# Kernel optimization log

Measured on AMD Instinct MI355X. Metric: run time of the kernel, lower is better.

The kernel has to match this reference:

```python
import jax, jax.numpy as jnp
import numpy as np

B, H, W, C = 8, 64, 64, 256
NH, WS, SS = 8, 8, 4
HD = C // NH          # head dim 32
N = WS * WS           # 64 tokens per window
NW = (H // WS) * (W // WS)  # 64 windows
MLP = 4 * C


def _rel_index():
    ch = np.arange(WS)
    coords = np.stack(np.meshgrid(ch, ch, indexing='ij')).reshape(2, -1)  # [2, N]
    rel = (coords[:, :, None] - coords[:, None, :]).transpose(1, 2, 0)   # [N, N, 2]
    rel[:, :, 0] += WS - 1
    rel[:, :, 1] += WS - 1
    rel[:, :, 0] *= 2 * WS - 1
    return jnp.asarray(rel.sum(-1))  # [N, N] indices into table

REL_IDX = _rel_index()


def _attn_mask():
    # standard Swin shifted-window mask: [nW, N, N] with 0 / -100
    img = np.zeros((H, W))
    slices = (slice(0, -WS), slice(-WS, -SS), slice(-SS, None))
    cnt = 0
    for hs in slices:
        for ws_ in slices:
            img[hs, ws_] = cnt
            cnt += 1
    m = img.reshape(H // WS, WS, W // WS, WS).transpose(0, 2, 1, 3).reshape(-1, N)
    diff = m[:, None, :] - m[:, :, None]
    return jnp.asarray(np.where(diff != 0, -100.0, 0.0).astype(np.float32))

MASK = _attn_mask()


def setup_inputs() -> dict:
    key = jax.random.key(0)
    ks = jax.random.split(key, 8)
    s = 0.02
    return {
        'hidden_states': jax.random.normal(ks[0], (B, H * W, C), jnp.float32),
        'ln1_g': jnp.ones((C,), jnp.float32),
        'ln1_b': jnp.zeros((C,), jnp.float32),
        'wq': jax.random.normal(ks[1], (C, C), jnp.float32) * s,
        'bq': jnp.zeros((C,), jnp.float32),
        'wk': jax.random.normal(ks[2], (C, C), jnp.float32) * s,
        'bk': jnp.zeros((C,), jnp.float32),
        'wv': jax.random.normal(ks[3], (C, C), jnp.float32) * s,
        'bv': jnp.zeros((C,), jnp.float32),
        'rel_table': jax.random.normal(ks[4], ((2 * WS - 1) ** 2, NH), jnp.float32) * s,
        'wo': jax.random.normal(ks[5], (C, C), jnp.float32) * s,
        'bo': jnp.zeros((C,), jnp.float32),
        'ln2_g': jnp.ones((C,), jnp.float32),
        'ln2_b': jnp.zeros((C,), jnp.float32),
        'w1': jax.random.normal(ks[6], (MLP, C), jnp.float32) * s,
        'b1': jnp.zeros((MLP,), jnp.float32),
        'w2': jax.random.normal(ks[7], (C, MLP), jnp.float32) * s,
        'b2': jnp.zeros((C,), jnp.float32),
    }


def _ln(x, g, b):
    mu = x.mean(-1, keepdims=True)
    var = x.var(-1, keepdims=True)
    return (x - mu) * jax.lax.rsqrt(var + 1e-5) * g + b


def reference(hidden_states, ln1_g, ln1_b, wq, bq, wk, bk, wv, bv, rel_table,
              wo, bo, ln2_g, ln2_b, w1, b1, w2, b2):
    shortcut = hidden_states
    x = _ln(hidden_states, ln1_g, ln1_b).reshape(B, H, W, C)
    # cyclic shift
    x = jnp.roll(x, (-SS, -SS), axis=(1, 2))
    # window partition -> [B*nW, N, C]
    xw = x.reshape(B, H // WS, WS, W // WS, WS, C).transpose(0, 1, 3, 2, 4, 5).reshape(-1, N, C)
    q = (xw @ wq.T + bq).reshape(-1, N, NH, HD).transpose(0, 2, 1, 3)
    k = (xw @ wk.T + bk).reshape(-1, N, NH, HD).transpose(0, 2, 1, 3)
    v = (xw @ wv.T + bv).reshape(-1, N, NH, HD).transpose(0, 2, 1, 3)
    scores = jnp.einsum('bhnd,bhmd->bhnm', q, k) / np.float32(np.sqrt(HD))
    bias = rel_table[REL_IDX]                 # [N, N, NH] gathered bias
    scores = scores + bias.transpose(2, 0, 1)[None]
    scores = scores.reshape(B, NW, NH, N, N) + MASK[None, :, None]
    probs = jax.nn.softmax(scores, axis=-1).reshape(-1, NH, N, N)
    ctx = jnp.einsum('bhnm,bhmd->bnhd', probs, v).reshape(-1, N, C)
    attn_out = ctx @ wo.T + bo                # SelfOutput dense
    # window reverse + reverse shift
    x = attn_out.reshape(B, H // WS, W // WS, WS, WS, C).transpose(0, 1, 3, 2, 4, 5).reshape(B, H, W, C)
    x = jnp.roll(x, (SS, SS), axis=(1, 2)).reshape(B, H * W, C)
    hidden = shortcut + x
    y = _ln(hidden, ln2_g, ln2_b)
    y = jax.nn.gelu(y @ w1.T + b1, approximate=False) @ w2.T + b2
    return hidden + y
```

## Files before the change

### kernel.cpp

```cpp
#include <hip/hip_runtime.h>
#include <hip/hip_bf16.h>
#include <math.h>

__device__ __forceinline__ unsigned short f2bf(float f) {
    union { float f; unsigned u; } c; c.f = f;
    unsigned r = c.u + 0x7fffu + ((c.u >> 16) & 1u);
    return (unsigned short)(r >> 16);
}
__device__ __forceinline__ float bfu(unsigned short u) {
    union { unsigned x; float f; } c; c.x = ((unsigned)u) << 16; return c.f;
}
__device__ __forceinline__ float gelu_t(float x) {
    float z = x * (1.59576912f + 0.07135481f * x * x);
    return x / (1.0f + __expf(-z));
}

typedef __bf16 bf16x8_t __attribute__((ext_vector_type(8)));
typedef float  f32x4_t  __attribute__((ext_vector_type(4)));
typedef unsigned short u16x8 __attribute__((ext_vector_type(8)));

#define AS1 __attribute__((address_space(1)))
#define AS3 __attribute__((address_space(3)))
__device__ __forceinline__ void g2lds16(const void* g, void* l) {
    __builtin_amdgcn_global_load_lds((const AS1 unsigned int*)g, (AS3 unsigned int*)l, 16, 0, 0);
}

__global__ void cvt_all(const float* __restrict__ wq, const float* __restrict__ wk,
                        const float* __restrict__ wv, const float* __restrict__ wo,
                        const float* __restrict__ w1, const float* __restrict__ w2,
                        unsigned short* __restrict__ wqkv_b, unsigned short* __restrict__ wo_b,
                        unsigned short* __restrict__ w1_b, unsigned short* __restrict__ w2_b) {
    int i = blockIdx.x * 256 + threadIdx.x;
    const float* src; unsigned short* dst; int base;
    if (i < 16384)       { src = wq; dst = wqkv_b;          base = 0; }
    else if (i < 32768)  { src = wk; dst = wqkv_b + 65536;  base = 16384; }
    else if (i < 49152)  { src = wv; dst = wqkv_b + 131072; base = 32768; }
    else if (i < 65536)  { src = wo; dst = wo_b;            base = 49152; }
    else if (i < 131072) { src = w1; dst = w1_b;            base = 65536; }
    else                 { src = w2; dst = w2_b;            base = 131072; }
    int j = (i - base) * 4;
    float4 v = *(const float4*)(src + j);
    ushort4 o = { f2bf(v.x), f2bf(v.y), f2bf(v.z), f2bf(v.w) };
    *(ushort4*)(dst + j) = o;
}

template<int GATHER, int BF16IN>
__global__ void ln_kernel(const void* __restrict__ xv, const float* __restrict__ g,
                          const float* __restrict__ b, unsigned short* __restrict__ out) {
    int row  = blockIdx.x * 4 + (threadIdx.x >> 6);
    int lane = threadIdx.x & 63;
    int src;
    if (GATHER) {
        int bb = row >> 12;
        int rem = row & 4095;
        int winid = rem >> 6, tok = rem & 63;
        int wi = winid >> 3, wj = winid & 7;
        int ii = tok >> 3,  jj = tok & 7;
        int hh = (wi * 8 + ii + 4) & 63;
        int ww = (wj * 8 + jj + 4) & 63;
        src = (bb << 12) + hh * 64 + ww;
    } else {
        src = row;
    }
    float4 v;
    if (BF16IN) {
        ushort4 u = *(const ushort4*)((const unsigned short*)xv + (size_t)src * 256 + lane * 4);
        v.x = bfu(u.x); v.y = bfu(u.y); v.z = bfu(u.z); v.w = bfu(u.w);
    } else {
        v = *(const float4*)((const float*)xv + (size_t)src * 256 + lane * 4);
    }
    float s  = v.x + v.y + v.z + v.w;
    float s2 = v.x*v.x + v.y*v.y + v.z*v.z + v.w*v.w;
    #pragma unroll
    for (int off = 32; off > 0; off >>= 1) {
        s  += __shfl_xor(s,  off, 64);
        s2 += __shfl_xor(s2, off, 64);
    }
    float mean = s * (1.0f / 256.0f);
    float var  = s2 * (1.0f / 256.0f) - mean * mean;
    float rstd = rsqrtf(var + 1e-5f);
    int c0 = lane * 4;
    float4 gg  = *(const float4*)(g + c0);
    float4 bb4 = *(const float4*)(b + c0);
    ushort4 o;
    o.x = f2bf((v.x - mean) * rstd * gg.x + bb4.x);
    o.y = f2bf((v.y - mean) * rstd * gg.y + bb4.y);
    o.z = f2bf((v.z - mean) * rstd * gg.z + bb4.z);
    o.w = f2bf((v.w - mean) * rstd * gg.w + bb4.w);
    *(ushort4*)(out + (size_t)row * 256 + c0) = o;
}

template<int MODE, int K>
__global__ __launch_bounds__(256, 4) void gemm_tile(
        const unsigned short* __restrict__ A,
        const unsigned short* __restrict__ Bw,
        const float* __restrict__ bias,
        int M, int N,
        unsigned short* __restrict__ obf,
        float* __restrict__ of32,
        const void* __restrict__ addp) {
    __shared__ __align__(16) char smem_raw[64 * 132 * 4];
    unsigned short* As = (unsigned short*)smem_raw;
    unsigned short* Bs = As + 128 * 64;
    float* cst = (float*)smem_raw;
    const int t = threadIdx.x;
    const int lane = t & 63, wave = t >> 6;
    const int m0 = blockIdx.x * 128, n0 = blockIdx.y * 128;
    const int wm = (wave >> 1) * 64, wn = (wave & 1) * 64;
    const int lr = lane & 15, kg = lane >> 4;

    f32x4_t acc[4][4];
    #pragma unroll
    for (int i = 0; i < 4; ++i)
        #pragma unroll
        for (int j = 0; j < 4; ++j) { acc[i][j][0]=0.f; acc[i][j][1]=0.f; acc[i][j][2]=0.f; acc[i][j][3]=0.f; }

    const int srow = t >> 3;
    const int sck  = (t & 7) * 8;
    const unsigned short* ga = A  + (size_t)(m0 + srow) * K + sck;
    const unsigned short* gb = Bw + (size_t)(n0 + srow) * K + sck;
    unsigned short* la = &As[t * 8];
    unsigned short* lb = &Bs[t * 8];

    #pragma unroll
    for (int k0 = 0; k0 < K; k0 += 64) {
        __syncthreads();
        #pragma unroll
        for (int i = 0; i < 4; ++i) {
            g2lds16(ga + (size_t)(i * 32) * K + k0, la + i * 2048);
            g2lds16(gb + (size_t)(i * 32) * K + k0, lb + i * 2048);
        }
        __syncthreads();
        #pragma unroll
        for (int ks = 0; ks < 64; ks += 32) {
            bf16x8_t af[4], bfr[4];
            #pragma unroll
            for (int i = 0; i < 4; ++i)
                af[i] = *(const bf16x8_t*)&As[(wm + i * 16 + lr) * 64 + ks + kg * 8];
            #pragma unroll
            for (int j = 0; j < 4; ++j)
                bfr[j] = *(const bf16x8_t*)&Bs[(wn + j * 16 + lr) * 64 + ks + kg * 8];
            #pragma unroll
            for (int i = 0; i < 4; ++i)
                #pragma unroll
                for (int j = 0; j < 4; ++j)
                    acc[i][j] = __builtin_amdgcn_mfma_f32_16x16x32_bf16(af[i], bfr[j], acc[i][j], 0, 0, 0);
        }
    }

    #pragma unroll
    for (int pass = 0; pass < 2; ++pass) {
        __syncthreads();
        if ((wave >> 1) == pass) {
            float* cw = cst + (kg * 4) * 132 + wn + lr;
            #pragma unroll
            for (int i = 0; i < 4; ++i)
                #pragma unroll
                for (int j = 0; j < 4; ++j)
                    #pragma unroll
                    for (int e = 0; e < 4; ++e)
                        cw[(i * 16 + e) * 132 + j * 16] = acc[i][j][e];
        }
        __syncthreads();
        const int rr = t >> 4;
        const int ch = t & 15;
        if (MODE == 0 || MODE == 1) {
            #pragma unroll
            for (int c = 0; c < 4; ++c) {
                int r = rr + c * 16;
                int grow = m0 + pass * 64 + r;
                const float* cr = cst + r * 132 + ch * 8;
                const float* bp = bias + n0 + ch * 8;
                float4 a   = *(const float4*)(cr);
                float4 b4  = *(const float4*)(cr + 4);
                float4 ba  = *(const float4*)(bp);
                float4 bb4 = *(const float4*)(bp + 4);
                float x0 = a.x + ba.x,  x1 = a.y + ba.y,  x2 = a.z + ba.z,  x3 = a.w + ba.w;
                float x4 = b4.x + bb4.x, x5 = b4.y + bb4.y, x6 = b4.z + bb4.z, x7 = b4.w + bb4.w;
                if (MODE == 1) {
                    x0 = gelu_t(x0); x1 = gelu_t(x1); x2 = gelu_t(x2); x3 = gelu_t(x3);
                    x4 = gelu_t(x4); x5 = gelu_t(x5); x6 = gelu_t(x6); x7 = gelu_t(x7);
                }
                u16x8 o = { f2bf(x0), f2bf(x1), f2bf(x2), f2bf(x3),
                            f2bf(x4), f2bf(x5), f2bf(x6), f2bf(x7) };
                *(u16x8*)(obf + (size_t)grow * N + n0 + ch * 8) = o;
            }
        } else if (MODE == 2) {
            #pragma unroll
            for (int c = 0; c < 4; ++c) {
                int r = rr + c * 16;
                int grow = m0 + pass * 64 + r;
                int bb_ = grow >> 12, rem = grow & 4095;
                int winid = rem >> 6, tok = rem & 63;
                int wi = winid >> 3, wj = winid & 7;
                int ii = tok >> 3,  jj = tok & 7;
                int hh = (wi * 8 + ii + 4) & 63;
                int ww = (wj * 8 + jj + 4) & 63;
                size_t drow = (size_t)(bb_ << 12) + hh * 64 + ww;
                const float* cr = cst + r * 132 + ch * 8;
                const float* bp = bias + n0 + ch * 8;
                const float* res = (const float*)addp + drow * N + n0 + ch * 8;
                float4 a   = *(const float4*)(cr);
                float4 b4  = *(const float4*)(cr + 4);
                float4 ba  = *(const float4*)(bp);
                float4 bb4 = *(const float4*)(bp + 4);
                float4 ra  = *(const float4*)(res);
                float4 rb  = *(const float4*)(res + 4);
                u16x8 o = { f2bf(a.x + ba.x + ra.x),  f2bf(a.y + ba.y + ra.y),
                            f2bf(a.z + ba.z + ra.z),  f2bf(a.w + ba.w + ra.w),
                            f2bf(b4.x + bb4.x + rb.x), f2bf(b4.y + bb4.y + rb.y),
                            f2bf(b4.z + bb4.z + rb.z), f2bf(b4.w + bb4.w + rb.w) };
                *(u16x8*)(obf + drow * N + n0 + ch * 8) = o;
            }
        } else {
            #pragma unroll
            for (int c = 0; c < 8; ++c) {
                int r = rr + (c & 3) * 16;
                int grow = m0 + pass * 64 + r;
                int chunk = ch + (c >> 2) * 16;
                const float* cr = cst + r * 132 + chunk * 4;
                const float* bp = bias + n0 + chunk * 4;
                const unsigned short* res = (const unsigned short*)addp + (size_t)grow * N + n0 + chunk * 4;
                float4 a  = *(const float4*)(cr);
                float4 ba = *(const float4*)(bp);
                ushort4 rv = *(const ushort4*)(res);
                float4 o1 = { bfu(rv.x) + a.x + ba.x,  bfu(rv.y) + a.y + ba.y,
                              bfu(rv.z) + a.z + ba.z,  bfu(rv.w) + a.w + ba.w };
                *(float4*)(of32 + (size_t)grow * N + n0 + chunk * 4) = o1;
            }
        }
    }
}

#define PR 72
#define VR 72
__global__ void __launch_bounds__(256) attn_mfma(
        const unsigned short* __restrict__ qkv,
        const float* __restrict__ relt,
        unsigned short* __restrict__ ctx) {
    __shared__ float rs[1800];
    __shared__ unsigned short Pl[4][64 * PR];
    __shared__ unsigned short Vt[4][32 * VR];

    int t = threadIdx.x;
    int lane = t & 63, wave = t >> 6;
    for (int i = t; i < 1800; i += 256) rs[i] = relt[i];
    __syncthreads();

    int wh = blockIdx.x * 4 + wave;
    int wg = wh >> 3, h = wh & 7;
    int win = wg & 63;
    int ln = lane & 15, quad = lane >> 4;

    unsigned short* P = &Pl[wave][0];
    unsigned short* V = &Vt[wave][0];
    const unsigned short* base = qkv + (size_t)wg * 64 * 768 + h * 32;

    union BF8 { bf16x8_t v; unsigned short s[8]; };
    {
        const bf16x8_t* vp = (const bf16x8_t*)(base + (size_t)lane * 768 + 512);
        BF8 vv[4];
        #pragma unroll
        for (int c = 0; c < 4; ++c) vv[c].v = vp[c];
        #pragma unroll
        for (int c = 0; c < 4; ++c)
            #pragma unroll
            for (int e = 0; e < 8; ++e)
                V[(c * 8 + e) * VR + lane] = vv[c].s[e];
    }

    bf16x8_t qa[4], kb[4];
    #pragma unroll
    for (int i = 0; i < 4; ++i)
        qa[i] = *(const bf16x8_t*)(base + (size_t)(i * 16 + ln) * 768 + quad * 8);
    #pragma unroll
    for (int j = 0; j < 4; ++j)
        kb[j] = *(const bf16x8_t*)(base + (size_t)(j * 16 + ln) * 768 + 256 + quad * 8);

    f32x4_t acc[4][4];
    #pragma unroll
    for (int i = 0; i < 4; ++i)
        #pragma unroll
        for (int j = 0; j < 4; ++j) { acc[i][j][0]=0.f; acc[i][j][1]=0.f; acc[i][j][2]=0.f; acc[i][j][3]=0.f; }
    #pragma unroll
    for (int i = 0; i < 4; ++i)
        #pragma unroll
        for (int j = 0; j < 4; ++j)
            acc[i][j] = __builtin_amdgcn_mfma_f32_16x16x32_bf16(qa[i], kb[j], acc[i][j], 0, 0, 0);

    const float scale = 0.17677669529663687f;
    int wi = win >> 3, wj = win & 7;
    int mjv = ln & 7;
    int regm[4], mi[4];
    #pragma unroll
    for (int j = 0; j < 4; ++j) {
        mi[j] = j * 2 + (ln >> 3);
        int hm = wi * 8 + mi[j], wm = wj * 8 + mjv;
        regm[j] = (hm < 56 ? 0 : (hm < 60 ? 1 : 2)) * 3 + (wm < 56 ? 0 : (wm < 60 ? 1 : 2));
    }
    float inv[4][4];
    #pragma unroll
    for (int i = 0; i < 4; ++i) {
        #pragma unroll
        for (int e = 0; e < 4; ++e) {
            int q = i * 16 + quad * 4 + e;
            int ti = q >> 3, tj = q & 7;
            int hn = wi * 8 + ti, wn = wj * 8 + tj;
            int regn = (hn < 56 ? 0 : (hn < 60 ? 1 : 2)) * 3 + (wn < 56 ? 0 : (wn < 60 ? 1 : 2));
            float sum = 0.f;
            #pragma unroll
            for (int j = 0; j < 4; ++j) {
                float bv = rs[((ti - mi[j] + 7) * 15 + (tj - mjv + 7)) * 8 + h];
                float s = acc[i][j][e] * scale + bv + (regm[j] != regn ? -100.f : 0.f);
                float p = __expf(s);
                sum += p;
                P[q * PR + j * 16 + ln] = f2bf(p);
            }
            #pragma unroll
            for (int off = 1; off < 16; off <<= 1) sum += __shfl_xor(sum, off, 64);
            inv[i][e] = 1.0f / sum;
        }
    }
    __syncthreads();

    bf16x8_t vb[2][2];
    #pragma unroll
    for (int jd = 0; jd < 2; ++jd)
        #pragma unroll
        for (int kc = 0; kc < 2; ++kc)
            vb[jd][kc] = *(const bf16x8_t*)&V[(jd * 16 + ln) * VR + kc * 32 + quad * 8];
    f32x4_t occ[4][2];
    #pragma unroll
    for (int i = 0; i < 4; ++i)
        #pragma unroll
        for (int jd = 0; jd < 2; ++jd) { occ[i][jd][0]=0.f; occ[i][jd][1]=0.f; occ[i][jd][2]=0.f; occ[i][jd][3]=0.f; }
    #pragma unroll
    for (int i = 0; i < 4; ++i) {
        #pragma unroll
        for (int kc = 0; kc < 2; ++kc) {
            bf16x8_t pf = *(const bf16x8_t*)&P[(i * 16 + ln) * PR + kc * 32 + quad * 8];
            occ[i][0] = __builtin_amdgcn_mfma_f32_16x16x32_bf16(pf, vb[0][kc], occ[i][0], 0, 0, 0);
            occ[i][1] = __builtin_amdgcn_mfma_f32_16x16x32_bf16(pf, vb[1][kc], occ[i][1], 0, 0, 0);
        }
    }

    unsigned short* cbase = ctx + (size_t)wg * 64 * 256 + h * 32;
    #pragma unroll
    for (int i = 0; i < 4; ++i)
        #pragma unroll
        for (int e = 0; e < 4; ++e) {
            int q = i * 16 + quad * 4 + e;
            #pragma unroll
            for (int jd = 0; jd < 2; ++jd)
                cbase[(size_t)q * 256 + jd * 16 + ln] = f2bf(occ[i][jd][e] * inv[i][e]);
        }
}

extern "C" void kernel_launch(void* const* d_in, const int* in_sizes, int n_in,
                              void* d_out, int out_size, void* d_ws, size_t ws_size,
                              hipStream_t stream) {
    const float* hs   = (const float*)d_in[0];
    const float* ln1g = (const float*)d_in[1];
    const float* ln1b = (const float*)d_in[2];
    const float* wq   = (const float*)d_in[3];
    const float* bq   = (const float*)d_in[4];
    const float* wk   = (const float*)d_in[5];
    const float* bk   = (const float*)d_in[6];
    const float* wv   = (const float*)d_in[7];
    const float* bv   = (const float*)d_in[8];
    const float* relt = (const float*)d_in[9];
    const float* wo   = (const float*)d_in[10];
    const float* bo   = (const float*)d_in[11];
    const float* ln2g = (const float*)d_in[12];
    const float* ln2b = (const float*)d_in[13];
    const float* w1   = (const float*)d_in[14];
    const float* b1   = (const float*)d_in[15];
    const float* w2   = (const float*)d_in[16];
    const float* b2   = (const float*)d_in[17];
    float* out = (float*)d_out;

    const size_t NTOK = 32768;
    size_t off = 0;
    auto carve = [&](size_t bytes) { void* p = (char*)d_ws + off; off += (bytes + 255) & ~(size_t)255; return p; };
    unsigned short* wqkv_b = (unsigned short*)carve(768ull * 256 * 2);
    unsigned short* wo_b   = (unsigned short*)carve(65536ull * 2);
    unsigned short* w1_b   = (unsigned short*)carve(262144ull * 2);
    unsigned short* w2_b   = (unsigned short*)carve(262144ull * 2);
    float*          bqkv   = (float*)carve(768ull * 4);
    unsigned short* hiddenb= (unsigned short*)carve(NTOK * 256 * 2);
    unsigned short* xw     = (unsigned short*)carve(NTOK * 256 * 2);
    unsigned short* qkvb   = (unsigned short*)carve(NTOK * 768 * 2);
    unsigned short* cx     = (unsigned short*)carve(NTOK * 256 * 2);
    unsigned short* h1 = qkvb;
    unsigned short* yb = xw;

    cvt_all<<<768, 256, 0, stream>>>(wq, wk, wv, wo, w1, w2, wqkv_b, wo_b, w1_b, w2_b);
    hipMemcpyAsync(bqkv,       bq, 256 * 4, hipMemcpyDeviceToDevice, stream);
    hipMemcpyAsync(bqkv + 256, bk, 256 * 4, hipMemcpyDeviceToDevice, stream);
    hipMemcpyAsync(bqkv + 512, bv, 256 * 4, hipMemcpyDeviceToDevice, stream);

    ln_kernel<1, 0><<<8192, 256, 0, stream>>>(hs, ln1g, ln1b, xw);

    gemm_tile<0, 256><<<dim3(256, 6), 256, 0, stream>>>(xw, wqkv_b, bqkv, 32768, 768, qkvb, nullptr, nullptr);

    attn_mfma<<<1024, 256, 0, stream>>>(qkvb, relt, cx);

    gemm_tile<2, 256><<<dim3(256, 2), 256, 0, stream>>>(cx, wo_b, bo, 32768, 256, hiddenb, nullptr, hs);

    ln_kernel<0, 1><<<8192, 256, 0, stream>>>(hiddenb, ln2g, ln2b, yb);

    gemm_tile<1, 256><<<dim3(256, 8), 256, 0, stream>>>(yb, w1_b, b1, 32768, 1024, h1, nullptr, nullptr);

    gemm_tile<3, 1024><<<dim3(256, 2), 256, 0, stream>>>(h1, w2_b, b2, 32768, 256, nullptr, out, hiddenb);
}
```

Measured before the change: 259.3 us.

## Double-buffer GEMM LDS tiles with K-step 32 to overlap loads and MFMA

The GEMM main loop now uses two LDS buffers with a K-tile of 32 instead of a single buffer with K-tile 64. The next tile's global-to-LDS loads are issued before the current tile's MFMAs, and there is one barrier per iteration instead of two. This is meant to hide global load latency behind compute. The cost is twice as many loop iterations and barriers per K. The waitcnt on the async LDS loads also depends on the barrier semantics.

```diff
diff --git a/kernel.cpp b/kernel.cpp
--- a/kernel.cpp
+++ b/kernel.cpp
@@ -100,8 +100,7 @@
         float* __restrict__ of32,
         const void* __restrict__ addp) {
     __shared__ __align__(16) char smem_raw[64 * 132 * 4];
-    unsigned short* As = (unsigned short*)smem_raw;
-    unsigned short* Bs = As + 128 * 64;
+    unsigned short* sm = (unsigned short*)smem_raw;
     float* cst = (float*)smem_raw;
     const int t = threadIdx.x;
     const int lane = t & 63, wave = t >> 6;
@@ -115,37 +114,47 @@
         #pragma unroll
         for (int j = 0; j < 4; ++j) { acc[i][j][0]=0.f; acc[i][j][1]=0.f; acc[i][j][2]=0.f; acc[i][j][3]=0.f; }
 
-    const int srow = t >> 3;
-    const int sck  = (t & 7) * 8;
-    const unsigned short* ga = A  + (size_t)(m0 + srow) * K + sck;
-    const unsigned short* gb = Bw + (size_t)(n0 + srow) * K + sck;
-    unsigned short* la = &As[t * 8];
-    unsigned short* lb = &Bs[t * 8];
-
-    #pragma unroll
-    for (int k0 = 0; k0 < K; k0 += 64) {
+    const unsigned short* ga = A  + (size_t)(m0 + (t >> 2)) * K + (t & 3) * 8;
+    const unsigned short* gb = Bw + (size_t)(n0 + (t >> 2)) * K + (t & 3) * 8;
+    unsigned short* lA = sm + t * 8;
+    unsigned short* lB = sm + 4096 + t * 8;
+
+    const int NT = K / 32;
+    {
+        g2lds16(ga,                     lA);
+        g2lds16(ga + (size_t)64 * K,    lA + 2048);
+        g2lds16(gb,                     lB);
+        g2lds16(gb + (size_t)64 * K,    lB + 2048);
+    }
+    __syncthreads();
+
+    #pragma unroll
+    for (int k = 0; k < NT; ++k) {
+        const int cur = k & 1;
+        if (k + 1 < NT) {
+            const int nx = cur ^ 1;
+            const unsigned short* gA = ga + (k + 1) * 32;
+            const unsigned short* gB = gb + (k + 1) * 32;
+            g2lds16(gA,                  lA + nx * 8192);
+            g2lds16(gA + (size_t)64 * K, lA + nx * 8192 + 2048);
+            g2lds16(gB,                  lB + nx * 8192);
+            g2lds16(gB + (size_t)64 * K, lB + nx * 8192 + 2048);
+        }
+        const unsigned short* Ab = sm + cur * 8192;
+        const unsigned short* Bb = Ab + 4096;
+        bf16x8_t af[4], bfr[4];
+        #pragma unroll
+        for (int i = 0; i < 4; ++i)
+            af[i] = *(const bf16x8_t*)&Ab[(wm + i * 16 + lr) * 32 + kg * 8];
+        #pragma unroll
+        for (int j = 0; j < 4; ++j)
+            bfr[j] = *(const bf16x8_t*)&Bb[(wn + j * 16 + lr) * 32 + kg * 8];
+        #pragma unroll
+        for (int i = 0; i < 4; ++i)
+            #pragma unroll
+            for (int j = 0; j < 4; ++j)
+                acc[i][j] = __builtin_amdgcn_mfma_f32_16x16x32_bf16(af[i], bfr[j], acc[i][j], 0, 0, 0);
         __syncthreads();
-        #pragma unroll
-        for (int i = 0; i < 4; ++i) {
-            g2lds16(ga + (size_t)(i * 32) * K + k0, la + i * 2048);
-            g2lds16(gb + (size_t)(i * 32) * K + k0, lb + i * 2048);
-        }
-        __syncthreads();
-        #pragma unroll
-        for (int ks = 0; ks < 64; ks += 32) {
-            bf16x8_t af[4], bfr[4];
-            #pragma unroll
-            for (int i = 0; i < 4; ++i)
-                af[i] = *(const bf16x8_t*)&As[(wm + i * 16 + lr) * 64 + ks + kg * 8];
-            #pragma unroll
-            for (int j = 0; j < 4; ++j)
-                bfr[j] = *(const bf16x8_t*)&Bs[(wn + j * 16 + lr) * 64 + ks + kg * 8];
-            #pragma unroll
-            for (int i = 0; i < 4; ++i)
-                #pragma unroll
-                for (int j = 0; j < 4; ++j)
-                    acc[i][j] = __builtin_amdgcn_mfma_f32_16x16x32_bf16(af[i], bfr[j], acc[i][j], 0, 0, 0);
-        }
     }
 
     #pragma unroll
```

Measured after the change: 251.6 us. 3.0% less time.
